# Kernel tuning notes

Hardware: AMD Instinct MI355X
Metric: run time of the kernel (lower is better)

The kernel has to match this reference:

```python
import jax, jax.numpy as jnp
import numpy as np

B, E, N, D = 4, 16, 1024, 512

def setup_inputs() -> dict:
    key = jax.random.key(0)
    kx, k1, k2, k3 = jax.random.split(key, 4)
    std = 1.0 / np.sqrt(D)
    x = jax.random.normal(kx, (B, E, N, D), dtype=jnp.float32)
    # weights: uniform(-std, std) per init_
    w1 = jax.random.uniform(k1, (E, D, D), dtype=jnp.float32, minval=-std, maxval=std)
    w2 = jax.random.uniform(k2, (E, D, D), dtype=jnp.float32, minval=-std, maxval=std)
    w3 = jax.random.uniform(k3, (E, D, D), dtype=jnp.float32, minval=-std, maxval=std)
    return {"x": x, "w1": w1, "w2": w2, "w3": w3}

def reference(x, w1, w2, w3):
    # per-expert projections: [b,e,n,d] x [e,d,h] -> [b,e,n,h]
    q = jnp.einsum('bend,edh->benh', x, w1)
    k = jnp.einsum('bend,edh->benh', x, w2)
    v = jnp.einsum('bend,edh->benh', x, w3)
    # global (n-reduced) attention: [b,e,h,d]
    atten = jnp.einsum('benh,bend->behd', q, k)
    atten = jax.nn.softmax(atten, axis=-1)
    # [b,e,n,h] x [b,e,h,h] -> [b,e,n,h]
    out = jnp.einsum('benh,behd->bend', v, atten)
    return out
```

## Files before the change

kernel.cpp:

```cpp
#include <hip/hip_runtime.h>
#include <stdint.h>

typedef unsigned short u16;
typedef __attribute__((ext_vector_type(8))) short bf16x8;
typedef __attribute__((ext_vector_type(4))) float floatx4;
typedef __attribute__((ext_vector_type(4))) u16 u16x4;

constexpr int B_ = 4, E_ = 16, N_ = 1024, D_ = 512;
constexpr int BE = B_ * E_;

__device__ __forceinline__ u16 f2bf(float f) {
    union { float f; uint32_t u; } v; v.f = f;
    return (u16)((v.u + 0x7fffu + ((v.u >> 16) & 1u)) >> 16);
}
__device__ __forceinline__ float bf2f(u16 h) {
    union { uint32_t u; float f; } v; v.u = ((uint32_t)h) << 16;
    return v.f;
}

#define GLDS(g, l) __builtin_amdgcn_global_load_lds( \
    (const __attribute__((address_space(1))) void*)(g), \
    (__attribute__((address_space(3))) void*)(l), 16, 0, 0)

__global__ __launch_bounds__(256)
void transpose_split(const float* __restrict__ in, u16* __restrict__ outH,
                     u16* __restrict__ outL, int R, int C)
{
    __shared__ float t[32][33];
    const int z = blockIdx.z;
    const float* ib = in + (size_t)z * R * C;
    u16* oh = outH + (size_t)z * R * C;
    u16* ol = outL + (size_t)z * R * C;
    const int r0 = blockIdx.y * 32, c0 = blockIdx.x * 32;
    const int t8 = threadIdx.x & 7, td = threadIdx.x >> 3;

    float4 v = *(const float4*)&ib[(size_t)(r0 + td) * C + c0 + t8 * 4];
    t[td][t8 * 4 + 0] = v.x;
    t[td][t8 * 4 + 1] = v.y;
    t[td][t8 * 4 + 2] = v.z;
    t[td][t8 * 4 + 3] = v.w;
    __syncthreads();

    u16x4 ph, pl;
    float w0 = t[t8 * 4 + 0][td], w1 = t[t8 * 4 + 1][td];
    float w2 = t[t8 * 4 + 2][td], w3 = t[t8 * 4 + 3][td];
    ph.x = f2bf(w0); pl.x = f2bf(w0 - bf2f(ph.x));
    ph.y = f2bf(w1); pl.y = f2bf(w1 - bf2f(ph.y));
    ph.z = f2bf(w2); pl.z = f2bf(w2 - bf2f(ph.z));
    ph.w = f2bf(w3); pl.w = f2bf(w3 - bf2f(ph.w));
    const size_t o = (size_t)(c0 + td) * R + r0 + t8 * 4;
    *(u16x4*)&oh[o] = ph;
    *(u16x4*)&ol[o] = pl;
}

__global__ __launch_bounds__(256)
void gemm_split3(const u16* __restrict__ Ah, const u16* __restrict__ Al,
                 int aMod, long aStride,
                 const u16* __restrict__ Bh, const u16* __restrict__ Bl,
                 int bMod, long bStride,
                 u16* __restrict__ Ch, u16* __restrict__ Cl,
                 float* __restrict__ Cf,
                 int M, int N, int K, int f32out)
{
    const int z = blockIdx.z;
    const long za = aMod ? (z % aMod) : z;
    const long zb = bMod ? (z % bMod) : z;
    const u16* pAh = Ah + za * aStride;
    const u16* pAl = Al + za * aStride;
    const u16* pBh = Bh + zb * bStride;
    const u16* pBl = Bl + zb * bStride;

    __shared__ __attribute__((aligned(16))) u16 sAh[128 * 32];
    __shared__ __attribute__((aligned(16))) u16 sAl[128 * 32];
    __shared__ __attribute__((aligned(16))) u16 sBh[128 * 32];
    __shared__ __attribute__((aligned(16))) u16 sBl[128 * 32];

    const int tid = threadIdx.x;
    const int wv = tid >> 6, ln = tid & 63;
    const int m0 = blockIdx.x * 128, n0 = blockIdx.y * 128;

    const int srow = wv * 16 + (ln >> 2);
    const int skcol = (ln & 3) * 8;
    const int lds0 = (wv * 16) * 32;
    const int lds1 = (64 + wv * 16) * 32;

    const int quad = ln >> 4, m16 = ln & 15;
    const int wm = wv >> 1, wn = wv & 1;

    floatx4 acc[4][4];
#pragma unroll
    for (int i = 0; i < 4; ++i)
#pragma unroll
        for (int j = 0; j < 4; ++j) acc[i][j] = (floatx4){0.f, 0.f, 0.f, 0.f};

    for (int k0 = 0; k0 < K; k0 += 32) {
        const long ka = k0 + skcol;
        GLDS(pAh + (long)(m0 + srow) * K + ka,      sAh + lds0);
        GLDS(pAh + (long)(m0 + 64 + srow) * K + ka, sAh + lds1);
        GLDS(pAl + (long)(m0 + srow) * K + ka,      sAl + lds0);
        GLDS(pAl + (long)(m0 + 64 + srow) * K + ka, sAl + lds1);
        GLDS(pBh + (long)(n0 + srow) * K + ka,      sBh + lds0);
        GLDS(pBh + (long)(n0 + 64 + srow) * K + ka, sBh + lds1);
        GLDS(pBl + (long)(n0 + srow) * K + ka,      sBl + lds0);
        GLDS(pBl + (long)(n0 + 64 + srow) * K + ka, sBl + lds1);
        __syncthreads();

        bf16x8 ah[4], al[4], bh[4], bl[4];
#pragma unroll
        for (int i = 0; i < 4; ++i) {
            const int off = (wm * 64 + i * 16 + m16) * 32 + quad * 8;
            ah[i] = *(const bf16x8*)&sAh[off];
            al[i] = *(const bf16x8*)&sAl[off];
        }
#pragma unroll
        for (int j = 0; j < 4; ++j) {
            const int off = (wn * 64 + j * 16 + m16) * 32 + quad * 8;
            bh[j] = *(const bf16x8*)&sBh[off];
            bl[j] = *(const bf16x8*)&sBl[off];
        }
#pragma unroll
        for (int i = 0; i < 4; ++i)
#pragma unroll
            for (int j = 0; j < 4; ++j) {
                acc[i][j] = __builtin_amdgcn_mfma_f32_16x16x32_bf16(ah[i], bh[j], acc[i][j], 0, 0, 0);
                acc[i][j] = __builtin_amdgcn_mfma_f32_16x16x32_bf16(ah[i], bl[j], acc[i][j], 0, 0, 0);
                acc[i][j] = __builtin_amdgcn_mfma_f32_16x16x32_bf16(al[i], bh[j], acc[i][j], 0, 0, 0);
            }
        __syncthreads();
    }

    const long cbase = (long)z * M * N;
#pragma unroll
    for (int i = 0; i < 4; ++i)
#pragma unroll
        for (int j = 0; j < 4; ++j) {
            const int col = n0 + wn * 64 + j * 16 + m16;
#pragma unroll
            for (int r = 0; r < 4; ++r) {
                const int row = m0 + wm * 64 + i * 16 + quad * 4 + r;
                const long idx = cbase + (long)row * N + col;
                const float v = acc[i][j][r];
                if (f32out) {
                    Cf[idx] = v;
                } else {
                    const u16 h = f2bf(v);
                    Ch[idx] = h;
                    Cl[idx] = f2bf(v - bf2f(h));
                }
            }
        }
}

template<int OTFA, int F32OUT>
__global__ __launch_bounds__(256)
void gemm_plain(const float* __restrict__ Qf, int qMod, long qStride,
                const u16* __restrict__ Pb, int pMod, long pStride,
                u16* __restrict__ Cb, float* __restrict__ Cf,
                int M, int N, int K)
{
    const int z = blockIdx.z;
    const float* pQ = Qf + (long)(qMod ? z % qMod : z) * qStride;
    const u16*  pP = Pb + (long)(pMod ? z % pMod : z) * pStride;

    __shared__ __attribute__((aligned(16))) u16 sA[128 * 32];
    __shared__ __attribute__((aligned(16))) u16 sB[128 * 32];

    const int tid = threadIdx.x;
    const int wv = tid >> 6, ln = tid & 63;
    const int m0 = blockIdx.x * 128, n0 = blockIdx.y * 128;

    u16* sBF = OTFA ? sB : sA;
    u16* sQ  = OTFA ? sA : sB;
    const int bfRow0 = OTFA ? n0 : m0;
    const int qRow0  = OTFA ? m0 : n0;

    const int srow = wv * 16 + (ln >> 2);
    const int skcol = (ln & 3) * 8;
    const int lds0 = (wv * 16) * 32;
    const int lds1 = (64 + wv * 16) * 32;

    const int frow = tid >> 3;
    const int fk4 = (tid & 7) * 4;

    const int quad = ln >> 4, m16 = ln & 15;
    const int wm = wv >> 1, wn = wv & 1;

    floatx4 acc[4][4];
#pragma unroll
    for (int i = 0; i < 4; ++i)
#pragma unroll
        for (int j = 0; j < 4; ++j) acc[i][j] = (floatx4){0.f, 0.f, 0.f, 0.f};

    for (int k0 = 0; k0 < K; k0 += 32) {
        GLDS(pP + (long)(bfRow0 + srow) * K + k0 + skcol,      sBF + lds0);
        GLDS(pP + (long)(bfRow0 + 64 + srow) * K + k0 + skcol, sBF + lds1);
#pragma unroll
        for (int r4 = 0; r4 < 4; ++r4) {
            const int row = r4 * 32 + frow;
            const float4 v = *(const float4*)&pQ[(long)(qRow0 + row) * K + k0 + fk4];
            u16x4 pk;
            pk.x = f2bf(v.x); pk.y = f2bf(v.y);
            pk.z = f2bf(v.z); pk.w = f2bf(v.w);
            *(u16x4*)&sQ[row * 32 + fk4] = pk;
        }
        __syncthreads();

        bf16x8 af[4], bg[4];
#pragma unroll
        for (int i = 0; i < 4; ++i)
            af[i] = *(const bf16x8*)&sA[(wm * 64 + i * 16 + m16) * 32 + quad * 8];
#pragma unroll
        for (int j = 0; j < 4; ++j)
            bg[j] = *(const bf16x8*)&sB[(wn * 64 + j * 16 + m16) * 32 + quad * 8];
#pragma unroll
        for (int i = 0; i < 4; ++i)
#pragma unroll
            for (int j = 0; j < 4; ++j)
                acc[i][j] = __builtin_amdgcn_mfma_f32_16x16x32_bf16(af[i], bg[j], acc[i][j], 0, 0, 0);
        __syncthreads();
    }

    const long cbase = (long)z * M * N;
#pragma unroll
    for (int i = 0; i < 4; ++i)
#pragma unroll
        for (int j = 0; j < 4; ++j) {
            const int col = n0 + wn * 64 + j * 16 + m16;
#pragma unroll
            for (int r = 0; r < 4; ++r) {
                const int row = m0 + wm * 64 + i * 16 + quad * 4 + r;
                const long idx = cbase + (long)row * N + col;
                if (F32OUT) Cf[idx] = acc[i][j][r];
                else        Cb[idx] = f2bf(acc[i][j][r]);
            }
        }
}

__global__ __launch_bounds__(128)
void softmax_col(const float* __restrict__ AT, u16* __restrict__ PT)
{
    const int z = blockIdx.x >> 2, gq = blockIdx.x & 3;
    const long base = (long)z * 512 * 512 + gq * 128 + threadIdx.x;
    const float* a = AT + base;
    u16* p = PT + base;

    float m = -1e30f, l = 0.f;
    for (int c = 0; c < 512; ++c) {
        const float v = a[(long)c * 512];
        const float mn = fmaxf(m, v);
        l = l * __expf(m - mn) + __expf(v - mn);
        m = mn;
    }
    const float inv = 1.0f / l;
    for (int c = 0; c < 512; ++c) {
        const float v = a[(long)c * 512];
        p[(long)c * 512] = f2bf(__expf(v - m) * inv);
    }
}

extern "C" void kernel_launch(void* const* d_in, const int* in_sizes, int n_in,
                              void* d_out, int out_size, void* d_ws, size_t ws_size,
                              hipStream_t stream)
{
    const float* x  = (const float*)d_in[0];
    const float* w1 = (const float*)d_in[1];
    const float* w2 = (const float*)d_in[2];
    const float* w3 = (const float*)d_in[3];

    char* O = (char*)d_out;
    char* W = (char*)d_ws;
    const size_t MB = 1ull << 20;

    u16* XhT  = (u16*)O;
    u16* XlT  = (u16*)(O + 64 * MB);
    u16* Gh   = (u16*)W;
    u16* Gl   = (u16*)(W + 32 * MB);
    u16* W2Th = (u16*)(O + 64 * MB);
    u16* W2Tl = (u16*)(O + 72 * MB);
    u16* Uh   = (u16*)O;
    u16* Ul   = (u16*)(O + 32 * MB);
    u16* W1Th = (u16*)W;
    u16* W1Tl = (u16*)(W + 8 * MB);
    float* AT = (float*)(O + 64 * MB);
    u16* PT   = (u16*)W;
    u16* MT   = (u16*)(W + 32 * MB);
    float* out = (float*)d_out;

    const long sXT = (long)512 * 1024;
    const long sSq = (long)512 * 512;

    transpose_split<<<dim3(16, 32, BE), 256, 0, stream>>>(x, XhT, XlT, 1024, 512);
    gemm_split3<<<dim3(4, 4, BE), 256, 0, stream>>>(
        XhT, XlT, 0, sXT, XhT, XlT, 0, sXT,
        Gh, Gl, nullptr, 512, 512, 1024, 0);
    transpose_split<<<dim3(16, 16, E_), 256, 0, stream>>>(w2, W2Th, W2Tl, 512, 512);
    gemm_split3<<<dim3(4, 4, BE), 256, 0, stream>>>(
        W2Th, W2Tl, E_, sSq, Gh, Gl, 0, sSq,
        Uh, Ul, nullptr, 512, 512, 512, 0);
    transpose_split<<<dim3(16, 16, E_), 256, 0, stream>>>(w1, W1Th, W1Tl, 512, 512);
    gemm_split3<<<dim3(4, 4, BE), 256, 0, stream>>>(
        Uh, Ul, 0, sSq, W1Th, W1Tl, E_, sSq,
        nullptr, nullptr, AT, 512, 512, 512, 1);
    softmax_col<<<dim3(BE * 4), 128, 0, stream>>>(AT, PT);
    gemm_plain<0, 0><<<dim3(4, 4, BE), 256, 0, stream>>>(
        w3, E_, sSq, PT, 0, sSq, MT, nullptr, 512, 512, 512);
    gemm_plain<1, 1><<<dim3(8, 4, BE), 256, 0, stream>>>(
        x, 0, (long)N_ * D_, MT, 0, sSq, nullptr, out, 1024, 512, 512);
}
```

Baseline: 745.6 us.

## Exploit Gram symmetry, fuse weight transposes, and use MFMA-fragment LDS layout

The X^T X Gram GEMM now launches only the 10 upper-triangular 128x128 tiles per batch and mirrors off-diagonal tiles on store. This removes about 37% of the largest split-bf16 GEMM's work. The two weight transpose/split kernels are merged into one launch, and workspace buffers are reshuffled to fit. The GEMM kernels also stage LDS in a fragment-major layout so each lane reads a contiguous 16 bytes, aiming to cut bank conflicts. In exchange, the mirrored stores are strided, uncoalesced writes.

```diff
diff --git a/kernel.cpp b/kernel.cpp
--- a/kernel.cpp
+++ b/kernel.cpp
@@ -5,6 +5,7 @@
 typedef __attribute__((ext_vector_type(8))) short bf16x8;
 typedef __attribute__((ext_vector_type(4))) float floatx4;
 typedef __attribute__((ext_vector_type(4))) u16 u16x4;
+typedef __attribute__((ext_vector_type(8))) u16 u16x8;
 
 constexpr int B_ = 4, E_ = 16, N_ = 1024, D_ = 512;
 constexpr int BE = B_ * E_;
@@ -54,13 +55,48 @@
 }
 
 __global__ __launch_bounds__(256)
+void transpose_split_w(const float* __restrict__ inA, u16* __restrict__ oAh, u16* __restrict__ oAl,
+                       const float* __restrict__ inB, u16* __restrict__ oBh, u16* __restrict__ oBl)
+{
+    __shared__ float t[32][33];
+    int z = blockIdx.z;
+    const float* in; u16* oh; u16* ol;
+    if (z < E_) { in = inA; oh = oAh; ol = oAl; }
+    else        { z -= E_; in = inB; oh = oBh; ol = oBl; }
+    const int R = 512, C = 512;
+    const float* ib = in + (size_t)z * R * C;
+    u16* ohz = oh + (size_t)z * R * C;
+    u16* olz = ol + (size_t)z * R * C;
+    const int r0 = blockIdx.y * 32, c0 = blockIdx.x * 32;
+    const int t8 = threadIdx.x & 7, td = threadIdx.x >> 3;
+
+    float4 v = *(const float4*)&ib[(size_t)(r0 + td) * C + c0 + t8 * 4];
+    t[td][t8 * 4 + 0] = v.x;
+    t[td][t8 * 4 + 1] = v.y;
+    t[td][t8 * 4 + 2] = v.z;
+    t[td][t8 * 4 + 3] = v.w;
+    __syncthreads();
+
+    u16x4 ph, pl;
+    float w0 = t[t8 * 4 + 0][td], w1 = t[t8 * 4 + 1][td];
+    float w2 = t[t8 * 4 + 2][td], w3 = t[t8 * 4 + 3][td];
+    ph.x = f2bf(w0); pl.x = f2bf(w0 - bf2f(ph.x));
+    ph.y = f2bf(w1); pl.y = f2bf(w1 - bf2f(ph.y));
+    ph.z = f2bf(w2); pl.z = f2bf(w2 - bf2f(ph.z));
+    ph.w = f2bf(w3); pl.w = f2bf(w3 - bf2f(ph.w));
+    const size_t o = (size_t)(c0 + td) * R + r0 + t8 * 4;
+    *(u16x4*)&ohz[o] = ph;
+    *(u16x4*)&olz[o] = pl;
+}
+
+__global__ __launch_bounds__(256)
 void gemm_split3(const u16* __restrict__ Ah, const u16* __restrict__ Al,
                  int aMod, long aStride,
                  const u16* __restrict__ Bh, const u16* __restrict__ Bl,
                  int bMod, long bStride,
                  u16* __restrict__ Ch, u16* __restrict__ Cl,
                  float* __restrict__ Cf,
-                 int M, int N, int K, int f32out)
+                 int M, int N, int K, int f32out, int sym)
 {
     const int z = blockIdx.z;
     const long za = aMod ? (z % aMod) : z;
@@ -70,21 +106,31 @@
     const u16* pBh = Bh + zb * bStride;
     const u16* pBl = Bl + zb * bStride;
 
-    __shared__ __attribute__((aligned(16))) u16 sAh[128 * 32];
-    __shared__ __attribute__((aligned(16))) u16 sAl[128 * 32];
-    __shared__ __attribute__((aligned(16))) u16 sBh[128 * 32];
-    __shared__ __attribute__((aligned(16))) u16 sBl[128 * 32];
+    __shared__ __attribute__((aligned(16))) u16 sA[8192];
+    __shared__ __attribute__((aligned(16))) u16 sB[8192];
 
     const int tid = threadIdx.x;
     const int wv = tid >> 6, ln = tid & 63;
-    const int m0 = blockIdx.x * 128, n0 = blockIdx.y * 128;
-
-    const int srow = wv * 16 + (ln >> 2);
-    const int skcol = (ln & 3) * 8;
-    const int lds0 = (wv * 16) * 32;
-    const int lds1 = (64 + wv * 16) * 32;
-
-    const int quad = ln >> 4, m16 = ln & 15;
+    const int lq = ln >> 4, lm = ln & 15;
+
+    int bi, bj;
+    if (sym) {
+        const int idx = blockIdx.x;
+        bi = (idx < 4) ? 0 : (idx < 7) ? 1 : (idx < 9) ? 2 : 3;
+        bj = idx - ((bi == 0) ? 0 : (bi == 1) ? 3 : (bi == 2) ? 5 : 6);
+    } else { bi = blockIdx.x; bj = blockIdx.y; }
+    const int m0 = bi * 128, n0 = bj * 128;
+
+    const u16* srcA[4];
+    const u16* srcB[4];
+#pragma unroll
+    for (int g = 0; g < 4; ++g) {
+        const int grp = wv * 4 + g;
+        const int row = (grp >> 3) * 64 + ((grp >> 1) & 3) * 16 + lm;
+        srcA[g] = ((grp & 1) ? pAl : pAh) + (long)(m0 + row) * K + lq * 8;
+        srcB[g] = ((grp & 1) ? pBl : pBh) + (long)(n0 + row) * K + lq * 8;
+    }
+
     const int wm = wv >> 1, wn = wv & 1;
 
     floatx4 acc[4][4];
@@ -94,29 +140,25 @@
         for (int j = 0; j < 4; ++j) acc[i][j] = (floatx4){0.f, 0.f, 0.f, 0.f};
 
     for (int k0 = 0; k0 < K; k0 += 32) {
-        const long ka = k0 + skcol;
-        GLDS(pAh + (long)(m0 + srow) * K + ka,      sAh + lds0);
-        GLDS(pAh + (long)(m0 + 64 + srow) * K + ka, sAh + lds1);
-        GLDS(pAl + (long)(m0 + srow) * K + ka,      sAl + lds0);
-        GLDS(pAl + (long)(m0 + 64 + srow) * K + ka, sAl + lds1);
-        GLDS(pBh + (long)(n0 + srow) * K + ka,      sBh + lds0);
-        GLDS(pBh + (long)(n0 + 64 + srow) * K + ka, sBh + lds1);
-        GLDS(pBl + (long)(n0 + srow) * K + ka,      sBl + lds0);
-        GLDS(pBl + (long)(n0 + 64 + srow) * K + ka, sBl + lds1);
+#pragma unroll
+        for (int g = 0; g < 4; ++g) {
+            GLDS(srcA[g] + k0, sA + (wv * 4 + g) * 512);
+            GLDS(srcB[g] + k0, sB + (wv * 4 + g) * 512);
+        }
         __syncthreads();
 
         bf16x8 ah[4], al[4], bh[4], bl[4];
 #pragma unroll
         for (int i = 0; i < 4; ++i) {
-            const int off = (wm * 64 + i * 16 + m16) * 32 + quad * 8;
-            ah[i] = *(const bf16x8*)&sAh[off];
-            al[i] = *(const bf16x8*)&sAl[off];
+            const int ga = (wm * 8 + i * 2) * 512 + ln * 8;
+            ah[i] = *(const bf16x8*)&sA[ga];
+            al[i] = *(const bf16x8*)&sA[ga + 512];
         }
 #pragma unroll
         for (int j = 0; j < 4; ++j) {
-            const int off = (wn * 64 + j * 16 + m16) * 32 + quad * 8;
-            bh[j] = *(const bf16x8*)&sBh[off];
-            bl[j] = *(const bf16x8*)&sBl[off];
+            const int gb = (wn * 8 + j * 2) * 512 + ln * 8;
+            bh[j] = *(const bf16x8*)&sB[gb];
+            bl[j] = *(const bf16x8*)&sB[gb + 512];
         }
 #pragma unroll
         for (int i = 0; i < 4; ++i)
@@ -134,18 +176,22 @@
     for (int i = 0; i < 4; ++i)
 #pragma unroll
         for (int j = 0; j < 4; ++j) {
-            const int col = n0 + wn * 64 + j * 16 + m16;
+            const int col = n0 + wn * 64 + j * 16 + lm;
 #pragma unroll
             for (int r = 0; r < 4; ++r) {
-                const int row = m0 + wm * 64 + i * 16 + quad * 4 + r;
-                const long idx = cbase + (long)row * N + col;
+                const int row = m0 + wm * 64 + i * 16 + lq * 4 + r;
                 const float v = acc[i][j][r];
                 if (f32out) {
-                    Cf[idx] = v;
+                    Cf[cbase + (long)row * N + col] = v;
                 } else {
                     const u16 h = f2bf(v);
-                    Ch[idx] = h;
-                    Cl[idx] = f2bf(v - bf2f(h));
+                    const u16 l = f2bf(v - bf2f(h));
+                    Ch[cbase + (long)row * N + col] = h;
+                    Cl[cbase + (long)row * N + col] = l;
+                    if (sym && bi != bj) {
+                        Ch[cbase + (long)col * N + row] = h;
+                        Cl[cbase + (long)col * N + row] = l;
+                    }
                 }
             }
         }
@@ -162,11 +208,12 @@
     const float* pQ = Qf + (long)(qMod ? z % qMod : z) * qStride;
     const u16*  pP = Pb + (long)(pMod ? z % pMod : z) * pStride;
 
-    __shared__ __attribute__((aligned(16))) u16 sA[128 * 32];
-    __shared__ __attribute__((aligned(16))) u16 sB[128 * 32];
+    __shared__ __attribute__((aligned(16))) u16 sA[4096];
+    __shared__ __attribute__((aligned(16))) u16 sB[4096];
 
     const int tid = threadIdx.x;
     const int wv = tid >> 6, ln = tid & 63;
+    const int lq = ln >> 4, lm = ln & 15;
     const int m0 = blockIdx.x * 128, n0 = blockIdx.y * 128;
 
     u16* sBF = OTFA ? sB : sA;
@@ -174,15 +221,23 @@
     const int bfRow0 = OTFA ? n0 : m0;
     const int qRow0  = OTFA ? m0 : n0;
 
-    const int srow = wv * 16 + (ln >> 2);
-    const int skcol = (ln & 3) * 8;
-    const int lds0 = (wv * 16) * 32;
-    const int lds1 = (64 + wv * 16) * 32;
-
-    const int frow = tid >> 3;
-    const int fk4 = (tid & 7) * 4;
-
-    const int quad = ln >> 4, m16 = ln & 15;
+    const u16* srcP[2];
+#pragma unroll
+    for (int g = 0; g < 2; ++g) {
+        const int grp = wv * 2 + g;
+        const int row = (grp >> 2) * 64 + (grp & 3) * 16 + lm;
+        srcP[g] = pP + (long)(bfRow0 + row) * K + lq * 8;
+    }
+
+    int orow[2], ok[2];
+#pragma unroll
+    for (int s = 0; s < 2; ++s) {
+        const int ci = tid + s * 256;
+        const int grp = ci >> 6, l = ci & 63;
+        orow[s] = qRow0 + (grp >> 2) * 64 + (grp & 3) * 16 + (l & 15);
+        ok[s]   = (l >> 4) * 8;
+    }
+
     const int wm = wv >> 1, wn = wv & 1;
 
     floatx4 acc[4][4];
@@ -192,26 +247,28 @@
         for (int j = 0; j < 4; ++j) acc[i][j] = (floatx4){0.f, 0.f, 0.f, 0.f};
 
     for (int k0 = 0; k0 < K; k0 += 32) {
-        GLDS(pP + (long)(bfRow0 + srow) * K + k0 + skcol,      sBF + lds0);
-        GLDS(pP + (long)(bfRow0 + 64 + srow) * K + k0 + skcol, sBF + lds1);
-#pragma unroll
-        for (int r4 = 0; r4 < 4; ++r4) {
-            const int row = r4 * 32 + frow;
-            const float4 v = *(const float4*)&pQ[(long)(qRow0 + row) * K + k0 + fk4];
-            u16x4 pk;
-            pk.x = f2bf(v.x); pk.y = f2bf(v.y);
-            pk.z = f2bf(v.z); pk.w = f2bf(v.w);
-            *(u16x4*)&sQ[row * 32 + fk4] = pk;
+#pragma unroll
+        for (int g = 0; g < 2; ++g)
+            GLDS(srcP[g] + k0, sBF + (wv * 2 + g) * 512);
+#pragma unroll
+        for (int s = 0; s < 2; ++s) {
+            const float* src = &pQ[(long)orow[s] * K + k0 + ok[s]];
+            const float4 v0 = *(const float4*)src;
+            const float4 v1 = *(const float4*)(src + 4);
+            u16x8 pk;
+            pk[0] = f2bf(v0.x); pk[1] = f2bf(v0.y); pk[2] = f2bf(v0.z); pk[3] = f2bf(v0.w);
+            pk[4] = f2bf(v1.x); pk[5] = f2bf(v1.y); pk[6] = f2bf(v1.z); pk[7] = f2bf(v1.w);
+            *(u16x8*)&sQ[(tid + s * 256) * 8] = pk;
         }
         __syncthreads();
 
         bf16x8 af[4], bg[4];
 #pragma unroll
         for (int i = 0; i < 4; ++i)
-            af[i] = *(const bf16x8*)&sA[(wm * 64 + i * 16 + m16) * 32 + quad * 8];
+            af[i] = *(const bf16x8*)&sA[(wm * 4 + i) * 512 + ln * 8];
 #pragma unroll
         for (int j = 0; j < 4; ++j)
-            bg[j] = *(const bf16x8*)&sB[(wn * 64 + j * 16 + m16) * 32 + quad * 8];
+            bg[j] = *(const bf16x8*)&sB[(wn * 4 + j) * 512 + ln * 8];
 #pragma unroll
         for (int i = 0; i < 4; ++i)
 #pragma unroll
@@ -225,10 +282,10 @@
     for (int i = 0; i < 4; ++i)
 #pragma unroll
         for (int j = 0; j < 4; ++j) {
-            const int col = n0 + wn * 64 + j * 16 + m16;
+            const int col = n0 + wn * 64 + j * 16 + lm;
 #pragma unroll
             for (int r = 0; r < 4; ++r) {
-                const int row = m0 + wm * 64 + i * 16 + quad * 4 + r;
+                const int row = m0 + wm * 64 + i * 16 + lq * 4 + r;
                 const long idx = cbase + (long)row * N + col;
                 if (F32OUT) Cf[idx] = acc[i][j][r];
                 else        Cb[idx] = f2bf(acc[i][j][r]);
@@ -277,30 +334,30 @@
     u16* Gl   = (u16*)(W + 32 * MB);
     u16* W2Th = (u16*)(O + 64 * MB);
     u16* W2Tl = (u16*)(O + 72 * MB);
+    u16* W1Th = (u16*)(O + 80 * MB);
+    u16* W1Tl = (u16*)(O + 88 * MB);
     u16* Uh   = (u16*)O;
     u16* Ul   = (u16*)(O + 32 * MB);
-    u16* W1Th = (u16*)W;
-    u16* W1Tl = (u16*)(W + 8 * MB);
-    float* AT = (float*)(O + 64 * MB);
-    u16* PT   = (u16*)W;
-    u16* MT   = (u16*)(W + 32 * MB);
+    float* AT = (float*)W;
+    u16* PT   = (u16*)(O + 64 * MB);
+    u16* MT   = (u16*)W;
     float* out = (float*)d_out;
 
     const long sXT = (long)512 * 1024;
     const long sSq = (long)512 * 512;
 
     transpose_split<<<dim3(16, 32, BE), 256, 0, stream>>>(x, XhT, XlT, 1024, 512);
-    gemm_split3<<<dim3(4, 4, BE), 256, 0, stream>>>(
+    gemm_split3<<<dim3(10, 1, BE), 256, 0, stream>>>(
         XhT, XlT, 0, sXT, XhT, XlT, 0, sXT,
-        Gh, Gl, nullptr, 512, 512, 1024, 0);
-    transpose_split<<<dim3(16, 16, E_), 256, 0, stream>>>(w2, W2Th, W2Tl, 512, 512);
+        Gh, Gl, nullptr, 512, 512, 1024, 0, 1);
+    transpose_split_w<<<dim3(16, 16, 2 * E_), 256, 0, stream>>>(
+        w2, W2Th, W2Tl, w1, W1Th, W1Tl);
     gemm_split3<<<dim3(4, 4, BE), 256, 0, stream>>>(
         W2Th, W2Tl, E_, sSq, Gh, Gl, 0, sSq,
-        Uh, Ul, nullptr, 512, 512, 512, 0);
-    transpose_split<<<dim3(16, 16, E_), 256, 0, stream>>>(w1, W1Th, W1Tl, 512, 512);
+        Uh, Ul, nullptr, 512, 512, 512, 0, 0);
     gemm_split3<<<dim3(4, 4, BE), 256, 0, stream>>>(
         Uh, Ul, 0, sSq, W1Th, W1Tl, E_, sSq,
-        nullptr, nullptr, AT, 512, 512, 512, 1);
+        nullptr, nullptr, AT, 512, 512, 512, 1, 0);
     softmax_col<<<dim3(BE * 4), 128, 0, stream>>>(AT, PT);
     gemm_plain<0, 0><<<dim3(4, 4, BE), 256, 0, stream>>>(
         w3, E_, sSq, PT, 0, sSq, MT, nullptr, 512, 512, 512);
```

After: 841.0 us. 1.13x slower.

## Remap GEMM blocks into batch-interleaved 1D grids, fuse weight transposes, precast w3

Applied to the files above, without the earlier changes.

Replaces the 3D grids of the split-bf16 and plain GEMMs with 1D grids. Block indices are remapped so that eight consecutive blocks share a tile position across different batch slices, with the aim of improving cache locality and the dispatch pattern across XCDs. Merges the w1 and w2 transpose-split launches into one kernel and casts w3 to bf16 ahead of time, so the M-stage GEMM loads both operands through global_load_lds instead of converting on the fly. The buffer layout is reshuffled to hold the extra weight copies, which adds more scratch traffic and memory use.

```diff
diff --git a/kernel.cpp b/kernel.cpp
--- a/kernel.cpp
+++ b/kernel.cpp
@@ -5,6 +5,7 @@
 typedef __attribute__((ext_vector_type(8))) short bf16x8;
 typedef __attribute__((ext_vector_type(4))) float floatx4;
 typedef __attribute__((ext_vector_type(4))) u16 u16x4;
+typedef __attribute__((ext_vector_type(8))) u16 u16x8;
 
 constexpr int B_ = 4, E_ = 16, N_ = 1024, D_ = 512;
 constexpr int BE = B_ * E_;
@@ -21,6 +22,7 @@
 #define GLDS(g, l) __builtin_amdgcn_global_load_lds( \
     (const __attribute__((address_space(1))) void*)(g), \
     (__attribute__((address_space(3))) void*)(l), 16, 0, 0)
+
 
 __global__ __launch_bounds__(256)
 void transpose_split(const float* __restrict__ in, u16* __restrict__ outH,
@@ -54,6 +56,54 @@
 }
 
 __global__ __launch_bounds__(256)
+void transpose_split_w(const float* __restrict__ inA, u16* __restrict__ oAh, u16* __restrict__ oAl,
+                       const float* __restrict__ inB, u16* __restrict__ oBh, u16* __restrict__ oBl)
+{
+    __shared__ float t[32][33];
+    int z = blockIdx.z;
+    const float* in; u16* oh; u16* ol;
+    if (z < E_) { in = inA; oh = oAh; ol = oAl; }
+    else        { z -= E_; in = inB; oh = oBh; ol = oBl; }
+    const int R = 512, C = 512;
+    const float* ib = in + (size_t)z * R * C;
+    u16* ohz = oh + (size_t)z * R * C;
+    u16* olz = ol + (size_t)z * R * C;
+    const int r0 = blockIdx.y * 32, c0 = blockIdx.x * 32;
+    const int t8 = threadIdx.x & 7, td = threadIdx.x >> 3;
+
+    float4 v = *(const float4*)&ib[(size_t)(r0 + td) * C + c0 + t8 * 4];
+    t[td][t8 * 4 + 0] = v.x;
+    t[td][t8 * 4 + 1] = v.y;
+    t[td][t8 * 4 + 2] = v.z;
+    t[td][t8 * 4 + 3] = v.w;
+    __syncthreads();
+
+    u16x4 ph, pl;
+    float w0 = t[t8 * 4 + 0][td], w1 = t[t8 * 4 + 1][td];
+    float w2 = t[t8 * 4 + 2][td], w3 = t[t8 * 4 + 3][td];
+    ph.x = f2bf(w0); pl.x = f2bf(w0 - bf2f(ph.x));
+    ph.y = f2bf(w1); pl.y = f2bf(w1 - bf2f(ph.y));
+    ph.z = f2bf(w2); pl.z = f2bf(w2 - bf2f(ph.z));
+    ph.w = f2bf(w3); pl.w = f2bf(w3 - bf2f(ph.w));
+    const size_t o = (size_t)(c0 + td) * R + r0 + t8 * 4;
+    *(u16x4*)&ohz[o] = ph;
+    *(u16x4*)&olz[o] = pl;
+}
+
+__global__ __launch_bounds__(256)
+void cast_bf16(const float* __restrict__ in, u16* __restrict__ out, long n4)
+{
+    const long stride = (long)gridDim.x * blockDim.x;
+    for (long i = (long)blockIdx.x * blockDim.x + threadIdx.x; i < n4; i += stride) {
+        const float4 v = *(const float4*)&in[i * 4];
+        u16x4 p;
+        p.x = f2bf(v.x); p.y = f2bf(v.y); p.z = f2bf(v.z); p.w = f2bf(v.w);
+        *(u16x4*)&out[i * 4] = p;
+    }
+}
+
+
+__global__ __launch_bounds__(256)
 void gemm_split3(const u16* __restrict__ Ah, const u16* __restrict__ Al,
                  int aMod, long aStride,
                  const u16* __restrict__ Bh, const u16* __restrict__ Bl,
@@ -62,7 +112,11 @@
                  float* __restrict__ Cf,
                  int M, int N, int K, int f32out)
 {
-    const int z = blockIdx.z;
+    const int lin = blockIdx.x;
+    const int rest = lin >> 3;
+    const int z = (lin & 7) + 8 * (rest >> 4);
+    const int bi = rest & 3, bj = (rest >> 2) & 3;
+
     const long za = aMod ? (z % aMod) : z;
     const long zb = bMod ? (z % bMod) : z;
     const u16* pAh = Ah + za * aStride;
@@ -77,7 +131,7 @@
 
     const int tid = threadIdx.x;
     const int wv = tid >> 6, ln = tid & 63;
-    const int m0 = blockIdx.x * 128, n0 = blockIdx.y * 128;
+    const int m0 = bi * 128, n0 = bj * 128;
 
     const int srow = wv * 16 + (ln >> 2);
     const int skcol = (ln & 3) * 8;
@@ -151,34 +205,103 @@
         }
 }
 
-template<int OTFA, int F32OUT>
-__global__ __launch_bounds__(256)
-void gemm_plain(const float* __restrict__ Qf, int qMod, long qStride,
-                const u16* __restrict__ Pb, int pMod, long pStride,
-                u16* __restrict__ Cb, float* __restrict__ Cf,
-                int M, int N, int K)
-{
-    const int z = blockIdx.z;
-    const float* pQ = Qf + (long)(qMod ? z % qMod : z) * qStride;
-    const u16*  pP = Pb + (long)(pMod ? z % pMod : z) * pStride;
+__global__ __launch_bounds__(256)
+void gemm_bb(const u16* __restrict__ Ab, int aMod, long aStride,
+             const u16* __restrict__ Bb, int bMod, long bStride,
+             u16* __restrict__ Cb, int M, int N, int K)
+{
+    const int lin = blockIdx.x;
+    const int rest = lin >> 3;
+    const int z = (lin & 7) + 8 * (rest >> 4);
+    const int bi = rest & 3, bj = (rest >> 2) & 3;
+
+    const u16* pA = Ab + (long)(aMod ? z % aMod : z) * aStride;
+    const u16* pB = Bb + (long)(bMod ? z % bMod : z) * bStride;
 
     __shared__ __attribute__((aligned(16))) u16 sA[128 * 32];
     __shared__ __attribute__((aligned(16))) u16 sB[128 * 32];
 
     const int tid = threadIdx.x;
     const int wv = tid >> 6, ln = tid & 63;
-    const int m0 = blockIdx.x * 128, n0 = blockIdx.y * 128;
-
-    u16* sBF = OTFA ? sB : sA;
-    u16* sQ  = OTFA ? sA : sB;
-    const int bfRow0 = OTFA ? n0 : m0;
-    const int qRow0  = OTFA ? m0 : n0;
+    const int m0 = bi * 128, n0 = bj * 128;
 
     const int srow = wv * 16 + (ln >> 2);
     const int skcol = (ln & 3) * 8;
     const int lds0 = (wv * 16) * 32;
     const int lds1 = (64 + wv * 16) * 32;
 
+    const int quad = ln >> 4, m16 = ln & 15;
+    const int wm = wv >> 1, wn = wv & 1;
+
+    floatx4 acc[4][4];
+#pragma unroll
+    for (int i = 0; i < 4; ++i)
+#pragma unroll
+        for (int j = 0; j < 4; ++j) acc[i][j] = (floatx4){0.f, 0.f, 0.f, 0.f};
+
+    for (int k0 = 0; k0 < K; k0 += 32) {
+        const long ka = k0 + skcol;
+        GLDS(pA + (long)(m0 + srow) * K + ka,      sA + lds0);
+        GLDS(pA + (long)(m0 + 64 + srow) * K + ka, sA + lds1);
+        GLDS(pB + (long)(n0 + srow) * K + ka,      sB + lds0);
+        GLDS(pB + (long)(n0 + 64 + srow) * K + ka, sB + lds1);
+        __syncthreads();
+
+        bf16x8 af[4], bg[4];
+#pragma unroll
+        for (int i = 0; i < 4; ++i)
+            af[i] = *(const bf16x8*)&sA[(wm * 64 + i * 16 + m16) * 32 + quad * 8];
+#pragma unroll
+        for (int j = 0; j < 4; ++j)
+            bg[j] = *(const bf16x8*)&sB[(wn * 64 + j * 16 + m16) * 32 + quad * 8];
+#pragma unroll
+        for (int i = 0; i < 4; ++i)
+#pragma unroll
+            for (int j = 0; j < 4; ++j)
+                acc[i][j] = __builtin_amdgcn_mfma_f32_16x16x32_bf16(af[i], bg[j], acc[i][j], 0, 0, 0);
+        __syncthreads();
+    }
+
+    const long cbase = (long)z * M * N;
+#pragma unroll
+    for (int i = 0; i < 4; ++i)
+#pragma unroll
+        for (int j = 0; j < 4; ++j) {
+            const int col = n0 + wn * 64 + j * 16 + m16;
+#pragma unroll
+            for (int r = 0; r < 4; ++r) {
+                const int row = m0 + wm * 64 + i * 16 + quad * 4 + r;
+                Cb[cbase + (long)row * N + col] = f2bf(acc[i][j][r]);
+            }
+        }
+}
+
+__global__ __launch_bounds__(256)
+void gemm_otfa(const float* __restrict__ Qf, long qStride,
+               const u16* __restrict__ Pb, long pStride,
+               float* __restrict__ Cf, int M, int N, int K)
+{
+    const int lin = blockIdx.x;
+    const int rest = lin >> 3;
+    const int z = (lin & 7) + 8 * (rest >> 5);
+    const int xy = rest & 31;
+    const int bi = xy & 7, bj = xy >> 3;
+
+    const float* pQ = Qf + (long)z * qStride;
+    const u16*  pP = Pb + (long)z * pStride;
+
+    __shared__ __attribute__((aligned(16))) u16 sA[128 * 32];
+    __shared__ __attribute__((aligned(16))) u16 sB[128 * 32];
+
+    const int tid = threadIdx.x;
+    const int wv = tid >> 6, ln = tid & 63;
+    const int m0 = bi * 128, n0 = bj * 128;
+
+    const int srow = wv * 16 + (ln >> 2);
+    const int skcol = (ln & 3) * 8;
+    const int lds0 = (wv * 16) * 32;
+    const int lds1 = (64 + wv * 16) * 32;
+
     const int frow = tid >> 3;
     const int fk4 = (tid & 7) * 4;
 
@@ -192,16 +315,16 @@
         for (int j = 0; j < 4; ++j) acc[i][j] = (floatx4){0.f, 0.f, 0.f, 0.f};
 
     for (int k0 = 0; k0 < K; k0 += 32) {
-        GLDS(pP + (long)(bfRow0 + srow) * K + k0 + skcol,      sBF + lds0);
-        GLDS(pP + (long)(bfRow0 + 64 + srow) * K + k0 + skcol, sBF + lds1);
+        GLDS(pP + (long)(n0 + srow) * K + k0 + skcol,      sB + lds0);
+        GLDS(pP + (long)(n0 + 64 + srow) * K + k0 + skcol, sB + lds1);
 #pragma unroll
         for (int r4 = 0; r4 < 4; ++r4) {
             const int row = r4 * 32 + frow;
-            const float4 v = *(const float4*)&pQ[(long)(qRow0 + row) * K + k0 + fk4];
+            const float4 v = *(const float4*)&pQ[(long)(m0 + row) * K + k0 + fk4];
             u16x4 pk;
             pk.x = f2bf(v.x); pk.y = f2bf(v.y);
             pk.z = f2bf(v.z); pk.w = f2bf(v.w);
-            *(u16x4*)&sQ[row * 32 + fk4] = pk;
+            *(u16x4*)&sA[row * 32 + fk4] = pk;
         }
         __syncthreads();
 
@@ -229,9 +352,7 @@
 #pragma unroll
             for (int r = 0; r < 4; ++r) {
                 const int row = m0 + wm * 64 + i * 16 + quad * 4 + r;
-                const long idx = cbase + (long)row * N + col;
-                if (F32OUT) Cf[idx] = acc[i][j][r];
-                else        Cb[idx] = f2bf(acc[i][j][r]);
+                Cf[cbase + (long)row * N + col] = acc[i][j][r];
             }
         }
 }
@@ -277,33 +398,35 @@
     u16* Gl   = (u16*)(W + 32 * MB);
     u16* W2Th = (u16*)(O + 64 * MB);
     u16* W2Tl = (u16*)(O + 72 * MB);
+    u16* W1Th = (u16*)(O + 80 * MB);
+    u16* W1Tl = (u16*)(O + 88 * MB);
+    u16* W3b  = (u16*)(O + 96 * MB);
     u16* Uh   = (u16*)O;
     u16* Ul   = (u16*)(O + 32 * MB);
-    u16* W1Th = (u16*)W;
-    u16* W1Tl = (u16*)(W + 8 * MB);
-    float* AT = (float*)(O + 64 * MB);
-    u16* PT   = (u16*)W;
-    u16* MT   = (u16*)(W + 32 * MB);
+    float* AT = (float*)W;
+    u16* PT   = (u16*)(O + 64 * MB);
+    u16* MT   = (u16*)W;
     float* out = (float*)d_out;
 
     const long sXT = (long)512 * 1024;
     const long sSq = (long)512 * 512;
 
     transpose_split<<<dim3(16, 32, BE), 256, 0, stream>>>(x, XhT, XlT, 1024, 512);
-    gemm_split3<<<dim3(4, 4, BE), 256, 0, stream>>>(
+    gemm_split3<<<dim3(1024), 256, 0, stream>>>(
         XhT, XlT, 0, sXT, XhT, XlT, 0, sXT,
         Gh, Gl, nullptr, 512, 512, 1024, 0);
-    transpose_split<<<dim3(16, 16, E_), 256, 0, stream>>>(w2, W2Th, W2Tl, 512, 512);
-    gemm_split3<<<dim3(4, 4, BE), 256, 0, stream>>>(
+    transpose_split_w<<<dim3(16, 16, 2 * E_), 256, 0, stream>>>(
+        w2, W2Th, W2Tl, w1, W1Th, W1Tl);
+    cast_bf16<<<dim3(1024), 256, 0, stream>>>(w3, W3b, (long)E_ * 512 * 512 / 4);
+    gemm_split3<<<dim3(1024), 256, 0, stream>>>(
         W2Th, W2Tl, E_, sSq, Gh, Gl, 0, sSq,
         Uh, Ul, nullptr, 512, 512, 512, 0);
-    transpose_split<<<dim3(16, 16, E_), 256, 0, stream>>>(w1, W1Th, W1Tl, 512, 512);
-    gemm_split3<<<dim3(4, 4, BE), 256, 0, stream>>>(
+    gemm_split3<<<dim3(1024), 256, 0, stream>>>(
         Uh, Ul, 0, sSq, W1Th, W1Tl, E_, sSq,
         nullptr, nullptr, AT, 512, 512, 512, 1);
     softmax_col<<<dim3(BE * 4), 128, 0, stream>>>(AT, PT);
-    gemm_plain<0, 0><<<dim3(4, 4, BE), 256, 0, stream>>>(
-        w3, E_, sSq, PT, 0, sSq, MT, nullptr, 512, 512, 512);
-    gemm_plain<1, 1><<<dim3(8, 4, BE), 256, 0, stream>>>(
-        x, 0, (long)N_ * D_, MT, 0, sSq, nullptr, out, 1024, 512, 512);
-}
+    gemm_bb<<<dim3(1024), 256, 0, stream>>>(
+        PT, 0, sSq, W3b, E_, sSq, MT, 512, 512, 512);
+    gemm_otfa<<<dim3(2048), 256, 0, stream>>>(
+        x, (long)N_ * D_, MT, sSq, out, 1024, 512, 512);
+}
```

Result: faster. 675.9 us (-9.4%).
